# Performance work log

Hardware: AMD Instinct MI355X
Metric: run time of the kernel (lower is better)

## Reference

```python
import jax, jax.numpy as jnp
import numpy as np

E, D_IN, D_OUT, N = 8, 1024, 1024, 8192

def setup_inputs() -> dict:
    key = jax.random.key(0)
    ks = jax.random.split(key, 5)
    s_in = 1.0 / np.sqrt(D_IN)
    x = jax.random.normal(ks[0], (N, D_IN), dtype=jnp.float32)
    We = jax.random.uniform(ks[1], (E, D_IN, D_OUT), dtype=jnp.float32, minval=-s_in, maxval=s_in)
    be = jax.random.uniform(ks[2], (E, D_OUT), dtype=jnp.float32, minval=-s_in, maxval=s_in)
    Wg = jax.random.uniform(ks[3], (D_IN, E), dtype=jnp.float32, minval=-s_in, maxval=s_in)
    bg = jax.random.uniform(ks[4], (E,), dtype=jnp.float32, minval=-s_in, maxval=s_in)
    return {"x": x, "We": We, "be": be, "Wg": Wg, "bg": bg}

def reference(x, We, be, Wg, bg):
    # experts_outputs: [N, E, D_OUT] (stacked per-expert Linear outputs)
    expert_out = jnp.einsum('ni,eio->neo', x, We) + be[None, :, :]
    # gate: softmax over experts, [N, E]
    gate = jax.nn.softmax(x @ Wg + bg, axis=1)
    # weighted combine (bmm of [N,1,E] x [N,E,D_OUT]) -> [N, D_OUT]
    return jnp.einsum('ne,neo->no', gate, expert_out)
```

## Files before the change

### kernel.cpp

```cpp
#include <hip/hip_runtime.h>
#include <hip/hip_bf16.h>
#include <cstdint>

#define NTOK 8192
#define DIN  1024
#define DOUT 1024
#define NEXP 8

typedef __attribute__((ext_vector_type(8)))  __bf16 bf16x8;
typedef __attribute__((ext_vector_type(4)))  float  f32x4;

__device__ __forceinline__ unsigned short f2bf(float f) {
    unsigned int u = __builtin_bit_cast(unsigned int, f);
    u += 0x7FFFu + ((u >> 16) & 1u);
    return (unsigned short)(u >> 16);
}

__device__ __forceinline__ void cp16(const void* gsrc, void* ldst) {
    __builtin_amdgcn_global_load_lds(
        (const __attribute__((address_space(1))) void*)gsrc,
        (__attribute__((address_space(3))) void*)ldst,
        16, 0, 0);
}

__global__ __launch_bounds__(256) void prep_kernel(
    const float* __restrict__ x, const float* __restrict__ We,
    const float* __restrict__ Wg, const float* __restrict__ bg,
    unsigned short* __restrict__ xb, unsigned short* __restrict__ wt,
    float* __restrict__ g)
{
    __shared__ float smem[12416];

    int t = threadIdx.x;

    if (blockIdx.x < 2048) {
        unsigned short* tile = (unsigned short*)smem;
        int b = blockIdx.x;
        int e  = b >> 8;
        int kt = (b >> 4) & 15;
        int ot = b & 15;

        const float* src = We + ((size_t)e << 20) + (size_t)(kt * 64) * DOUT + ot * 64;
        unsigned short* dst = wt + ((size_t)e << 20) + (size_t)(ot * 64) * DIN + kt * 64;

        int kl = t >> 2;
        int og = (t & 3) * 16;
#pragma unroll
        for (int c = 0; c < 4; ++c) {
            int o = og + c * 4;
            float4 v = *(const float4*)&src[(size_t)kl * DOUT + o];
            ushort4 u;
            u.x = f2bf(v.x); u.y = f2bf(v.y); u.z = f2bf(v.z); u.w = f2bf(v.w);
            *(ushort4*)&tile[kl * 72 + o] = u;
        }
        __syncthreads();
        int ol = t >> 2;
        int kg = (t & 3) * 16;
        unsigned short tmp[16];
#pragma unroll
        for (int i = 0; i < 16; ++i) tmp[i] = tile[(kg + i) * 72 + ol];
        *(uint4*)&dst[(size_t)ol * DIN + kg]     = *(uint4*)&tmp[0];
        *(uint4*)&dst[(size_t)ol * DIN + kg + 8] = *(uint4*)&tmp[8];
    } else {
        float* WgL = smem;
        float* xL  = smem + 8192;
        int n0 = (blockIdx.x - 2048) * 32;

#pragma unroll
        for (int q = 0; q < 8; ++q) {
            int fidx = q * 256 + t;
            int k  = fidx >> 1;
            int eh = (fidx & 1) * 4;
            float4 v = *(const float4*)&Wg[(size_t)k * 8 + eh];
            WgL[(eh + 0) * 1024 + k] = v.x;
            WgL[(eh + 1) * 1024 + k] = v.y;
            WgL[(eh + 2) * 1024 + k] = v.z;
            WgL[(eh + 3) * 1024 + k] = v.w;
        }

        int tt = t & 31;
        int e  = t >> 5;
        float acc = 0.f;

        for (int c = 0; c < 8; ++c) {
            int kb = c * 128;
#pragma unroll
            for (int q = 0; q < 4; ++q) {
                int fidx = q * 256 + t;
                int row = fidx >> 5;
                int kk  = (fidx & 31) * 4;
                float4 v = *(const float4*)&x[(size_t)(n0 + row) * DIN + kb + kk];
                ushort4 u;
                u.x = f2bf(v.x); u.y = f2bf(v.y); u.z = f2bf(v.z); u.w = f2bf(v.w);
                *(ushort4*)&xb[(size_t)(n0 + row) * DIN + kb + kk] = u;
                *(float4*)&xL[row * 132 + kk] = v;
            }
            __syncthreads();
#pragma unroll
            for (int kk = 0; kk < 128; kk += 4) {
                float4 xv = *(const float4*)&xL[tt * 132 + kk];
                float4 wv = *(const float4*)&WgL[e * 1024 + kb + kk];
                acc += xv.x * wv.x + xv.y * wv.y + xv.z * wv.z + xv.w * wv.w;
            }
            __syncthreads();
        }

        float* lg = xL;
        lg[tt * 8 + e] = acc + bg[e];
        __syncthreads();
        if (t < 32) {
            float l[8];
#pragma unroll
            for (int i = 0; i < 8; ++i) l[i] = lg[t * 8 + i];
            float m = l[0];
#pragma unroll
            for (int i = 1; i < 8; ++i) m = fmaxf(m, l[i]);
            float s = 0.f;
#pragma unroll
            for (int i = 0; i < 8; ++i) { l[i] = __expf(l[i] - m); s += l[i]; }
            float inv = 1.0f / s;
            float4 p0 = make_float4(l[0]*inv, l[1]*inv, l[2]*inv, l[3]*inv);
            float4 p1 = make_float4(l[4]*inv, l[5]*inv, l[6]*inv, l[7]*inv);
            *(float4*)&g[(size_t)(n0 + tt) * 8]     = p0;
            *(float4*)&g[(size_t)(n0 + tt) * 8 + 4] = p1;
        }
    }
}

__global__ __launch_bounds__(256, 2) void moe_gemm_kernel(
    const unsigned short* __restrict__ xb,
    const unsigned short* __restrict__ wt,
    const float* __restrict__ g,
    const float* __restrict__ be,
    float* __restrict__ out)
{
    __shared__ unsigned short lA0[128 * 64];
    __shared__ unsigned short lA1[128 * 64];
    __shared__ unsigned short lB0[128 * 64];
    __shared__ unsigned short lB1[128 * 64];

    int bid = blockIdx.x;
    int bm = (bid & 7) * 8 + ((bid >> 3) & 7);
    int bn = bid >> 6;
    int tid = threadIdx.x;
    int lane = tid & 63;
    int wave = tid >> 6;
    int wm = wave >> 1;
    int wn = wave & 1;

    const unsigned short* aBase = xb + (size_t)(bm * 128) * DIN;
    const unsigned short* bBase0 = wt + (size_t)(bn * 128) * DIN;

    int rowS = wave * 8 + (lane >> 3);
    int k8   = (((lane & 7) ^ (lane >> 3)) * 8);
    int rA   = lane & 15;
    int quad = lane >> 4;
    int swz  = rA & 7;

    f32x4 outAcc[4][4] = {};

#pragma unroll 1
    for (int e = 0; e < NEXP; ++e) {
        f32x4 acc[4][4] = {};
        const unsigned short* bBase = bBase0 + ((size_t)e << 20);

#pragma unroll 1
        for (int kt = 0; kt < 8; ++kt) {
            int kb = kt * 128;
            __syncthreads();
#pragma unroll
            for (int j = 0; j < 4; ++j) {
                int row = j * 32 + rowS;
                size_t so0 = (size_t)row * DIN + kb + k8;
                size_t so1 = so0 + 64;
                int dst = j * 2048 + wave * 512;
                cp16(aBase + so0, &lA0[dst]);
                cp16(aBase + so1, &lA1[dst]);
                cp16(bBase + so0, &lB0[dst]);
                cp16(bBase + so1, &lB1[dst]);
            }
            __syncthreads();
#pragma unroll
            for (int ks = 0; ks < 2; ++ks) {
                int kc = ks * 4 + quad;
                int kp = (kc ^ swz) * 8;
                bf16x8 af[4], bfr[4];
#pragma unroll
                for (int i = 0; i < 4; ++i)
                    af[i] = *(const bf16x8*)&lA0[(wm * 64 + i * 16 + rA) * 64 + kp];
#pragma unroll
                for (int j = 0; j < 4; ++j)
                    bfr[j] = *(const bf16x8*)&lB0[(wn * 64 + j * 16 + rA) * 64 + kp];
#pragma unroll
                for (int i = 0; i < 4; ++i)
#pragma unroll
                    for (int j = 0; j < 4; ++j)
                        acc[i][j] = __builtin_amdgcn_mfma_f32_16x16x32_bf16(
                            af[i], bfr[j], acc[i][j], 0, 0, 0);
#pragma unroll
                for (int i = 0; i < 4; ++i)
                    af[i] = *(const bf16x8*)&lA1[(wm * 64 + i * 16 + rA) * 64 + kp];
#pragma unroll
                for (int j = 0; j < 4; ++j)
                    bfr[j] = *(const bf16x8*)&lB1[(wn * 64 + j * 16 + rA) * 64 + kp];
#pragma unroll
                for (int i = 0; i < 4; ++i)
#pragma unroll
                    for (int j = 0; j < 4; ++j)
                        acc[i][j] = __builtin_amdgcn_mfma_f32_16x16x32_bf16(
                            af[i], bfr[j], acc[i][j], 0, 0, 0);
            }
        }

        float bv[4];
#pragma unroll
        for (int j = 0; j < 4; ++j)
            bv[j] = be[(size_t)e * DOUT + bn * 128 + wn * 64 + j * 16 + rA];
#pragma unroll
        for (int i = 0; i < 4; ++i) {
            int rbase = bm * 128 + wm * 64 + i * 16 + quad * 4;
            float g0 = g[(size_t)(rbase + 0) * 8 + e];
            float g1 = g[(size_t)(rbase + 1) * 8 + e];
            float g2 = g[(size_t)(rbase + 2) * 8 + e];
            float g3 = g[(size_t)(rbase + 3) * 8 + e];
#pragma unroll
            for (int j = 0; j < 4; ++j) {
                outAcc[i][j].x += g0 * (acc[i][j].x + bv[j]);
                outAcc[i][j].y += g1 * (acc[i][j].y + bv[j]);
                outAcc[i][j].z += g2 * (acc[i][j].z + bv[j]);
                outAcc[i][j].w += g3 * (acc[i][j].w + bv[j]);
            }
        }
    }

#pragma unroll
    for (int i = 0; i < 4; ++i) {
        int rowb = bm * 128 + wm * 64 + i * 16 + quad * 4;
#pragma unroll
        for (int j = 0; j < 4; ++j) {
            int col = bn * 128 + wn * 64 + j * 16 + rA;
            out[(size_t)(rowb + 0) * DOUT + col] = outAcc[i][j].x;
            out[(size_t)(rowb + 1) * DOUT + col] = outAcc[i][j].y;
            out[(size_t)(rowb + 2) * DOUT + col] = outAcc[i][j].z;
            out[(size_t)(rowb + 3) * DOUT + col] = outAcc[i][j].w;
        }
    }
}

extern "C" void kernel_launch(void* const* d_in, const int* in_sizes, int n_in,
                              void* d_out, int out_size, void* d_ws, size_t ws_size,
                              hipStream_t stream)
{
    const float* x  = (const float*)d_in[0];
    const float* We = (const float*)d_in[1];
    const float* be = (const float*)d_in[2];
    const float* Wg = (const float*)d_in[3];
    const float* bg = (const float*)d_in[4];
    float* out = (float*)d_out;

    unsigned short* xb = (unsigned short*)d_ws;
    unsigned short* wt = xb + (size_t)NTOK * DIN;
    float* g = (float*)(wt + (size_t)NEXP * DOUT * DIN);

    prep_kernel<<<2048 + 256, 256, 0, stream>>>(x, We, Wg, bg, xb, wt, g);
    moe_gemm_kernel<<<(NTOK / 128) * (DOUT / 128), 256, 0, stream>>>(xb, wt, g, be, out);
}
```

Before: 262.5 us.

## Triple-buffer LDS pipeline with 256x128 tiles and 512-thread blocks

Restructures the MoE GEMM main loop into a 3-stage LDS ring buffer that issues direct-to-LDS loads two k-steps ahead, with explicit vmcnt waits and raw s_barrier in place of __syncthreads. The block tile grows to 256x128 with 8 waves, which halves the grid and changes the block-to-tile mapping. Each k-step now covers 64 columns instead of 128 and is split into two MFMA phases raised with s_setprio. The aim is to hide global load latency behind MFMA work and raise B-tile reuse. In exchange, LDS use rises to about 144 KB, so only one block can fit per CU and the stated launch bound of 2 cannot be met. The hand-written vmcnt accounting is also fragile.

```diff
diff --git a/kernel.cpp b/kernel.cpp
--- a/kernel.cpp
+++ b/kernel.cpp
@@ -22,6 +22,8 @@
         (__attribute__((address_space(3))) void*)ldst,
         16, 0, 0);
 }
+
+#define BAR() asm volatile("s_barrier" ::: "memory")
 
 __global__ __launch_bounds__(256) void prep_kernel(
     const float* __restrict__ x, const float* __restrict__ We,
@@ -127,89 +129,133 @@
     }
 }
 
-__global__ __launch_bounds__(256, 2) void moe_gemm_kernel(
+__global__ __launch_bounds__(512, 2) void moe_gemm_kernel(
     const unsigned short* __restrict__ xb,
     const unsigned short* __restrict__ wt,
     const float* __restrict__ g,
     const float* __restrict__ be,
     float* __restrict__ out)
 {
-    __shared__ unsigned short lA0[128 * 64];
-    __shared__ unsigned short lA1[128 * 64];
-    __shared__ unsigned short lB0[128 * 64];
-    __shared__ unsigned short lB1[128 * 64];
+    __shared__ unsigned short lA[3][256 * 64];
+    __shared__ unsigned short lB[3][128 * 64];
 
     int bid = blockIdx.x;
-    int bm = (bid & 7) * 8 + ((bid >> 3) & 7);
-    int bn = bid >> 6;
-    int tid = threadIdx.x;
+    int wg = ((bid & 7) << 5) | (bid >> 3);
+    int bm = wg >> 3;
+    int bn = wg & 7;
+
+    int tid  = threadIdx.x;
     int lane = tid & 63;
     int wave = tid >> 6;
     int wm = wave >> 1;
     int wn = wave & 1;
 
-    const unsigned short* aBase = xb + (size_t)(bm * 128) * DIN;
-    const unsigned short* bBase0 = wt + (size_t)(bn * 128) * DIN;
-
-    int rowS = wave * 8 + (lane >> 3);
-    int k8   = (((lane & 7) ^ (lane >> 3)) * 8);
     int rA   = lane & 15;
     int quad = lane >> 4;
     int swz  = rA & 7;
+    int kp0  = ((quad    ) ^ swz) << 3;
+    int kp1  = ((quad + 4) ^ swz) << 3;
+    int aRowB = (wm * 64 + rA) * 64;
+    int bRowB = (wn * 64 + rA) * 64;
+
+    int srcOff = (tid >> 3) * DIN + (((tid & 7) ^ ((tid >> 3) & 7)) << 3);
+    int wOff   = wave * 512;
+
+    const unsigned short* aB = xb + (size_t)(bm * 256) * DIN;
+    const unsigned short* bB = wt + (size_t)(bn * 128) * DIN;
+
+#pragma unroll
+    for (int r = 0; r < 4; ++r)
+        cp16(aB + (size_t)(r * 64) * DIN + srcOff, &lA[0][r * 4096 + wOff]);
+#pragma unroll
+    for (int r = 0; r < 2; ++r)
+        cp16(bB + (size_t)(r * 64) * DIN + srcOff, &lB[0][r * 4096 + wOff]);
+#pragma unroll
+    for (int r = 0; r < 4; ++r)
+        cp16(aB + (size_t)(r * 64) * DIN + 64 + srcOff, &lA[1][r * 4096 + wOff]);
+#pragma unroll
+    for (int r = 0; r < 2; ++r)
+        cp16(bB + (size_t)(r * 64) * DIN + 64 + srcOff, &lB[1][r * 4096 + wOff]);
 
     f32x4 outAcc[4][4] = {};
+    f32x4 acc[4][4] = {};
+    const f32x4 fz = {0.f, 0.f, 0.f, 0.f};
+
+    int cur = 0;
 
 #pragma unroll 1
     for (int e = 0; e < NEXP; ++e) {
-        f32x4 acc[4][4] = {};
-        const unsigned short* bBase = bBase0 + ((size_t)e << 20);
-
 #pragma unroll 1
-        for (int kt = 0; kt < 8; ++kt) {
-            int kb = kt * 128;
-            __syncthreads();
+        for (int kt = 0; kt < 16; ++kt) {
+            int t = (e << 4) + kt;
+            int nxt = cur ? (cur - 1) : 2;
+
+            if (t < 126) {
+                int tt = t + 2;
+                const unsigned short* a2 = aB + ((tt & 15) << 6);
+#pragma unroll
+                for (int r = 0; r < 4; ++r)
+                    cp16(a2 + (size_t)(r * 64) * DIN + srcOff, &lA[nxt][r * 4096 + wOff]);
+                asm volatile("s_waitcnt vmcnt(10)" ::: "memory");
+            } else if (t == 126) {
+                asm volatile("s_waitcnt vmcnt(6)" ::: "memory");
+            } else {
+                asm volatile("s_waitcnt vmcnt(0)" ::: "memory");
+            }
+            BAR();
+
+            bf16x8 bfr[4][2], afA[2][2];
 #pragma unroll
             for (int j = 0; j < 4; ++j) {
-                int row = j * 32 + rowS;
-                size_t so0 = (size_t)row * DIN + kb + k8;
-                size_t so1 = so0 + 64;
-                int dst = j * 2048 + wave * 512;
-                cp16(aBase + so0, &lA0[dst]);
-                cp16(aBase + so1, &lA1[dst]);
-                cp16(bBase + so0, &lB0[dst]);
-                cp16(bBase + so1, &lB1[dst]);
-            }
-            __syncthreads();
-#pragma unroll
-            for (int ks = 0; ks < 2; ++ks) {
-                int kc = ks * 4 + quad;
-                int kp = (kc ^ swz) * 8;
-                bf16x8 af[4], bfr[4];
-#pragma unroll
-                for (int i = 0; i < 4; ++i)
-                    af[i] = *(const bf16x8*)&lA0[(wm * 64 + i * 16 + rA) * 64 + kp];
-#pragma unroll
-                for (int j = 0; j < 4; ++j)
-                    bfr[j] = *(const bf16x8*)&lB0[(wn * 64 + j * 16 + rA) * 64 + kp];
-#pragma unroll
-                for (int i = 0; i < 4; ++i)
-#pragma unroll
-                    for (int j = 0; j < 4; ++j)
-                        acc[i][j] = __builtin_amdgcn_mfma_f32_16x16x32_bf16(
-                            af[i], bfr[j], acc[i][j], 0, 0, 0);
-#pragma unroll
-                for (int i = 0; i < 4; ++i)
-                    af[i] = *(const bf16x8*)&lA1[(wm * 64 + i * 16 + rA) * 64 + kp];
-#pragma unroll
-                for (int j = 0; j < 4; ++j)
-                    bfr[j] = *(const bf16x8*)&lB1[(wn * 64 + j * 16 + rA) * 64 + kp];
-#pragma unroll
-                for (int i = 0; i < 4; ++i)
-#pragma unroll
-                    for (int j = 0; j < 4; ++j)
-                        acc[i][j] = __builtin_amdgcn_mfma_f32_16x16x32_bf16(
-                            af[i], bfr[j], acc[i][j], 0, 0, 0);
-            }
+                bfr[j][0] = *(const bf16x8*)&lB[cur][bRowB + j * 1024 + kp0];
+                bfr[j][1] = *(const bf16x8*)&lB[cur][bRowB + j * 1024 + kp1];
+            }
+#pragma unroll
+            for (int i = 0; i < 2; ++i) {
+                afA[i][0] = *(const bf16x8*)&lA[cur][aRowB + i * 1024 + kp0];
+                afA[i][1] = *(const bf16x8*)&lA[cur][aRowB + i * 1024 + kp1];
+            }
+            if (t < 126) {
+                int tt = t + 2;
+                const unsigned short* b2 = wt + ((size_t)(tt >> 4) << 20)
+                                         + (size_t)(bn * 128) * DIN + ((tt & 15) << 6);
+#pragma unroll
+                for (int r = 0; r < 2; ++r)
+                    cp16(b2 + (size_t)(r * 64) * DIN + srcOff, &lB[nxt][r * 4096 + wOff]);
+            }
+            __builtin_amdgcn_s_setprio(1);
+#pragma unroll
+            for (int i = 0; i < 2; ++i)
+#pragma unroll
+                for (int j = 0; j < 4; ++j) {
+                    acc[i][j] = __builtin_amdgcn_mfma_f32_16x16x32_bf16(
+                        afA[i][0], bfr[j][0], acc[i][j], 0, 0, 0);
+                    acc[i][j] = __builtin_amdgcn_mfma_f32_16x16x32_bf16(
+                        afA[i][1], bfr[j][1], acc[i][j], 0, 0, 0);
+                }
+            __builtin_amdgcn_s_setprio(0);
+            BAR();
+
+            bf16x8 afB[2][2];
+#pragma unroll
+            for (int i = 0; i < 2; ++i) {
+                afB[i][0] = *(const bf16x8*)&lA[cur][aRowB + (i + 2) * 1024 + kp0];
+                afB[i][1] = *(const bf16x8*)&lA[cur][aRowB + (i + 2) * 1024 + kp1];
+            }
+            __builtin_amdgcn_s_setprio(1);
+#pragma unroll
+            for (int i = 0; i < 2; ++i)
+#pragma unroll
+                for (int j = 0; j < 4; ++j) {
+                    acc[i + 2][j] = __builtin_amdgcn_mfma_f32_16x16x32_bf16(
+                        afB[i][0], bfr[j][0], acc[i + 2][j], 0, 0, 0);
+                    acc[i + 2][j] = __builtin_amdgcn_mfma_f32_16x16x32_bf16(
+                        afB[i][1], bfr[j][1], acc[i + 2][j], 0, 0, 0);
+                }
+            __builtin_amdgcn_s_setprio(0);
+            BAR();
+
+            cur = (cur == 2) ? 0 : cur + 1;
         }
 
         float bv[4];
@@ -218,7 +264,7 @@
             bv[j] = be[(size_t)e * DOUT + bn * 128 + wn * 64 + j * 16 + rA];
 #pragma unroll
         for (int i = 0; i < 4; ++i) {
-            int rbase = bm * 128 + wm * 64 + i * 16 + quad * 4;
+            int rbase = bm * 256 + wm * 64 + i * 16 + quad * 4;
             float g0 = g[(size_t)(rbase + 0) * 8 + e];
             float g1 = g[(size_t)(rbase + 1) * 8 + e];
             float g2 = g[(size_t)(rbase + 2) * 8 + e];
@@ -229,13 +275,14 @@
                 outAcc[i][j].y += g1 * (acc[i][j].y + bv[j]);
                 outAcc[i][j].z += g2 * (acc[i][j].z + bv[j]);
                 outAcc[i][j].w += g3 * (acc[i][j].w + bv[j]);
+                acc[i][j] = fz;
             }
         }
     }
 
 #pragma unroll
     for (int i = 0; i < 4; ++i) {
-        int rowb = bm * 128 + wm * 64 + i * 16 + quad * 4;
+        int rowb = bm * 256 + wm * 64 + i * 16 + quad * 4;
 #pragma unroll
         for (int j = 0; j < 4; ++j) {
             int col = bn * 128 + wn * 64 + j * 16 + rA;
@@ -263,5 +310,5 @@
     float* g = (float*)(wt + (size_t)NEXP * DOUT * DIN);
 
     prep_kernel<<<2048 + 256, 256, 0, stream>>>(x, We, Wg, bg, xb, wt, g);
-    moe_gemm_kernel<<<(NTOK / 128) * (DOUT / 128), 256, 0, stream>>>(xb, wt, g, be, out);
-}
+    moe_gemm_kernel<<<(NTOK / 256) * (DOUT / 128), 512, 0, stream>>>(xb, wt, g, be, out);
+}
```

New measurement: 287.3 us. +9.4%, slower.

## Restructure MoE GEMM to compute all experts per tile with double-buffered prefetch

Applied to the files above, without the earlier changes.

The GEMM kernel now uses 512-thread blocks, each covering 256 tokens by 32 output columns across all 8 experts at once. The K loop runs over 64-wide slices with double-buffered LDS and prefetches the next slice while the current one computes. Previously each expert was a separate K loop with two barriers per step. The A fragments are reused across 8 expert B fragments, and the gated combine moves to a single epilogue. The block-to-tile mapping is XCD-aware and s_setprio is set around the MFMA runs. The cost is 8x4 accumulators per wave, so register pressure is high and spills or lower occupancy are possible.

```diff
diff --git a/kernel.cpp b/kernel.cpp
--- a/kernel.cpp
+++ b/kernel.cpp
@@ -22,6 +22,8 @@
         (__attribute__((address_space(3))) void*)ldst,
         16, 0, 0);
 }
+
+#define BAR() asm volatile("s_barrier" ::: "memory")
 
 __global__ __launch_bounds__(256) void prep_kernel(
     const float* __restrict__ x, const float* __restrict__ We,
@@ -127,122 +129,124 @@
     }
 }
 
-__global__ __launch_bounds__(256, 2) void moe_gemm_kernel(
+__global__ __launch_bounds__(512, 2) void moe_gemm_kernel(
     const unsigned short* __restrict__ xb,
     const unsigned short* __restrict__ wt,
     const float* __restrict__ g,
     const float* __restrict__ be,
     float* __restrict__ out)
 {
-    __shared__ unsigned short lA0[128 * 64];
-    __shared__ unsigned short lA1[128 * 64];
-    __shared__ unsigned short lB0[128 * 64];
-    __shared__ unsigned short lB1[128 * 64];
+    __shared__ unsigned short lA[2][256 * 64];
+    __shared__ unsigned short lB[2][256 * 64];
 
     int bid = blockIdx.x;
-    int bm = (bid & 7) * 8 + ((bid >> 3) & 7);
-    int bn = bid >> 6;
-    int tid = threadIdx.x;
+    int xcd = bid & 7;
+    int wl  = bid >> 3;
+    int bn  = xcd * 4 + (wl & 3);
+    int bm  = wl >> 2;
+
+    int tid  = threadIdx.x;
     int lane = tid & 63;
     int wave = tid >> 6;
     int wm = wave >> 1;
     int wn = wave & 1;
 
-    const unsigned short* aBase = xb + (size_t)(bm * 128) * DIN;
-    const unsigned short* bBase0 = wt + (size_t)(bn * 128) * DIN;
-
-    int rowS = wave * 8 + (lane >> 3);
-    int k8   = (((lane & 7) ^ (lane >> 3)) * 8);
     int rA   = lane & 15;
     int quad = lane >> 4;
     int swz  = rA & 7;
 
-    f32x4 outAcc[4][4] = {};
+    int srow   = tid >> 3;
+    int schunk = ((tid & 7) ^ (srow & 7)) << 3;
+    int wOff   = wave * 512;
+
+    const unsigned short* aP0 = xb + (size_t)(bm * 256 + srow) * DIN + schunk;
+    const unsigned short* aP1 = aP0 + (size_t)64 * DIN;
+    const unsigned short* aP2 = aP0 + (size_t)128 * DIN;
+    const unsigned short* aP3 = aP0 + (size_t)192 * DIN;
+    int eHi = srow >> 5;
+    int col = srow & 31;
+    const unsigned short* bP0 = wt + ((size_t)(0 + eHi) << 20) + (size_t)(bn * 32 + col) * DIN + schunk;
+    const unsigned short* bP1 = wt + ((size_t)(2 + eHi) << 20) + (size_t)(bn * 32 + col) * DIN + schunk;
+    const unsigned short* bP2 = wt + ((size_t)(4 + eHi) << 20) + (size_t)(bn * 32 + col) * DIN + schunk;
+    const unsigned short* bP3 = wt + ((size_t)(6 + eHi) << 20) + (size_t)(bn * 32 + col) * DIN + schunk;
+
+    cp16(aP0, &lA[0][0 * 4096 + wOff]);
+    cp16(aP1, &lA[0][1 * 4096 + wOff]);
+    cp16(aP2, &lA[0][2 * 4096 + wOff]);
+    cp16(aP3, &lA[0][3 * 4096 + wOff]);
+    cp16(bP0, &lB[0][0 * 4096 + wOff]);
+    cp16(bP1, &lB[0][1 * 4096 + wOff]);
+    cp16(bP2, &lB[0][2 * 4096 + wOff]);
+    cp16(bP3, &lB[0][3 * 4096 + wOff]);
+
+    f32x4 acc[8][4] = {};
+
+    asm volatile("s_waitcnt vmcnt(0)" ::: "memory");
+    BAR();
 
 #pragma unroll 1
-    for (int e = 0; e < NEXP; ++e) {
-        f32x4 acc[4][4] = {};
-        const unsigned short* bBase = bBase0 + ((size_t)e << 20);
-
-#pragma unroll 1
-        for (int kt = 0; kt < 8; ++kt) {
-            int kb = kt * 128;
-            __syncthreads();
-#pragma unroll
-            for (int j = 0; j < 4; ++j) {
-                int row = j * 32 + rowS;
-                size_t so0 = (size_t)row * DIN + kb + k8;
-                size_t so1 = so0 + 64;
-                int dst = j * 2048 + wave * 512;
-                cp16(aBase + so0, &lA0[dst]);
-                cp16(aBase + so1, &lA1[dst]);
-                cp16(bBase + so0, &lB0[dst]);
-                cp16(bBase + so1, &lB1[dst]);
+    for (int t = 0; t < 16; ++t) {
+        if (t < 15) {
+            int nb = (t + 1) & 1;
+            size_t ko = (size_t)(t + 1) * 64;
+            cp16(aP0 + ko, &lA[nb][0 * 4096 + wOff]);
+            cp16(aP1 + ko, &lA[nb][1 * 4096 + wOff]);
+            cp16(aP2 + ko, &lA[nb][2 * 4096 + wOff]);
+            cp16(aP3 + ko, &lA[nb][3 * 4096 + wOff]);
+            cp16(bP0 + ko, &lB[nb][0 * 4096 + wOff]);
+            cp16(bP1 + ko, &lB[nb][1 * 4096 + wOff]);
+            cp16(bP2 + ko, &lB[nb][2 * 4096 + wOff]);
+            cp16(bP3 + ko, &lB[nb][3 * 4096 + wOff]);
+        }
+
+        const unsigned short* A = lA[t & 1];
+        const unsigned short* B = lB[t & 1];
+#pragma unroll
+        for (int h = 0; h < 2; ++h) {
+            int kp = ((quad + h * 4) ^ swz) << 3;
+            bf16x8 af[4];
+#pragma unroll
+            for (int i = 0; i < 4; ++i)
+                af[i] = *(const bf16x8*)&A[(wm * 64 + i * 16 + rA) * 64 + kp];
+            __builtin_amdgcn_s_setprio(1);
+#pragma unroll
+            for (int e = 0; e < 8; ++e) {
+                bf16x8 bfr = *(const bf16x8*)&B[(e * 32 + wn * 16 + rA) * 64 + kp];
+#pragma unroll
+                for (int i = 0; i < 4; ++i)
+                    acc[e][i] = __builtin_amdgcn_mfma_f32_16x16x32_bf16(
+                        af[i], bfr, acc[e][i], 0, 0, 0);
             }
-            __syncthreads();
-#pragma unroll
-            for (int ks = 0; ks < 2; ++ks) {
-                int kc = ks * 4 + quad;
-                int kp = (kc ^ swz) * 8;
-                bf16x8 af[4], bfr[4];
-#pragma unroll
-                for (int i = 0; i < 4; ++i)
-                    af[i] = *(const bf16x8*)&lA0[(wm * 64 + i * 16 + rA) * 64 + kp];
-#pragma unroll
-                for (int j = 0; j < 4; ++j)
-                    bfr[j] = *(const bf16x8*)&lB0[(wn * 64 + j * 16 + rA) * 64 + kp];
-#pragma unroll
-                for (int i = 0; i < 4; ++i)
-#pragma unroll
-                    for (int j = 0; j < 4; ++j)
-                        acc[i][j] = __builtin_amdgcn_mfma_f32_16x16x32_bf16(
-                            af[i], bfr[j], acc[i][j], 0, 0, 0);
-#pragma unroll
-                for (int i = 0; i < 4; ++i)
-                    af[i] = *(const bf16x8*)&lA1[(wm * 64 + i * 16 + rA) * 64 + kp];
-#pragma unroll
-                for (int j = 0; j < 4; ++j)
-                    bfr[j] = *(const bf16x8*)&lB1[(wn * 64 + j * 16 + rA) * 64 + kp];
-#pragma unroll
-                for (int i = 0; i < 4; ++i)
-#pragma unroll
-                    for (int j = 0; j < 4; ++j)
-                        acc[i][j] = __builtin_amdgcn_mfma_f32_16x16x32_bf16(
-                            af[i], bfr[j], acc[i][j], 0, 0, 0);
-            }
-        }
-
-        float bv[4];
-#pragma unroll
-        for (int j = 0; j < 4; ++j)
-            bv[j] = be[(size_t)e * DOUT + bn * 128 + wn * 64 + j * 16 + rA];
-#pragma unroll
-        for (int i = 0; i < 4; ++i) {
-            int rbase = bm * 128 + wm * 64 + i * 16 + quad * 4;
-            float g0 = g[(size_t)(rbase + 0) * 8 + e];
-            float g1 = g[(size_t)(rbase + 1) * 8 + e];
-            float g2 = g[(size_t)(rbase + 2) * 8 + e];
-            float g3 = g[(size_t)(rbase + 3) * 8 + e];
-#pragma unroll
-            for (int j = 0; j < 4; ++j) {
-                outAcc[i][j].x += g0 * (acc[i][j].x + bv[j]);
-                outAcc[i][j].y += g1 * (acc[i][j].y + bv[j]);
-                outAcc[i][j].z += g2 * (acc[i][j].z + bv[j]);
-                outAcc[i][j].w += g3 * (acc[i][j].w + bv[j]);
-            }
+            __builtin_amdgcn_s_setprio(0);
+        }
+
+        if (t < 15) {
+            asm volatile("s_waitcnt vmcnt(0)" ::: "memory");
+            BAR();
         }
     }
 
+    int colg = bn * 32 + wn * 16 + rA;
+    float bcol[8];
+#pragma unroll
+    for (int e = 0; e < 8; ++e) bcol[e] = be[(size_t)e * DOUT + colg];
 #pragma unroll
     for (int i = 0; i < 4; ++i) {
-        int rowb = bm * 128 + wm * 64 + i * 16 + quad * 4;
-#pragma unroll
-        for (int j = 0; j < 4; ++j) {
-            int col = bn * 128 + wn * 64 + j * 16 + rA;
-            out[(size_t)(rowb + 0) * DOUT + col] = outAcc[i][j].x;
-            out[(size_t)(rowb + 1) * DOUT + col] = outAcc[i][j].y;
-            out[(size_t)(rowb + 2) * DOUT + col] = outAcc[i][j].z;
-            out[(size_t)(rowb + 3) * DOUT + col] = outAcc[i][j].w;
+        int rbase = bm * 256 + wm * 64 + i * 16 + quad * 4;
+#pragma unroll
+        for (int rr = 0; rr < 4; ++rr) {
+            const float* gp = &g[(size_t)(rbase + rr) * 8];
+            float4 g0 = *(const float4*)gp;
+            float4 g1 = *(const float4*)(gp + 4);
+            float s = g0.x * (acc[0][i][rr] + bcol[0])
+                    + g0.y * (acc[1][i][rr] + bcol[1])
+                    + g0.z * (acc[2][i][rr] + bcol[2])
+                    + g0.w * (acc[3][i][rr] + bcol[3])
+                    + g1.x * (acc[4][i][rr] + bcol[4])
+                    + g1.y * (acc[5][i][rr] + bcol[5])
+                    + g1.z * (acc[6][i][rr] + bcol[6])
+                    + g1.w * (acc[7][i][rr] + bcol[7]);
+            out[(size_t)(rbase + rr) * DOUT + colg] = s;
         }
     }
 }
@@ -263,5 +267,5 @@
     float* g = (float*)(wt + (size_t)NEXP * DOUT * DIN);
 
     prep_kernel<<<2048 + 256, 256, 0, stream>>>(x, We, Wg, bg, xb, wt, g);
-    moe_gemm_kernel<<<(NTOK / 128) * (DOUT / 128), 256, 0, stream>>>(xb, wt, g, be, out);
-}
+    moe_gemm_kernel<<<(NTOK / 256) * (DOUT / 32), 512, 0, stream>>>(xb, wt, g, be, out);
+}
```

Measured after the change: 267.1 us. Within noise of the previous version (+1.8%).
